# Performance work log

Hardware: AMD Instinct MI355X
Metric: run time of the kernel (lower is better)

## Reference

```python
import jax, jax.numpy as jnp
import numpy as np
from jax import lax

# db4 decomposition low-pass filter (pywt convention, ascending index)
DEC_LO = np.array([-0.010597401784997278, 0.032883011666982945, 0.030841381835986965,
                   -0.18703481171888114, -0.02798376941698385, 0.6308807679295904,
                   0.7148465705525415, 0.23037781330885523], dtype=np.float32)
L = 8
REC_LO = DEC_LO[::-1].copy()
DEC_HI = (REC_LO * ((-1.0) ** (np.arange(L) + 1))).astype(np.float32)
REC_HI = DEC_HI[::-1].copy()


def _dwt_last(x, lo, hi):
    """Single-level DWT along last axis, pywt 'symmetric' mode.
    Returns (cA, cD), each (..., (N+L-1)//2)."""
    ext = jnp.pad(x, [(0, 0)] * (x.ndim - 1) + [(L - 1, L - 1)], mode='symmetric')[..., 1:]
    z = ext.reshape(-1, 1, ext.shape[-1])
    # correlation with flipped filter == true convolution
    k = jnp.stack([lo[::-1], hi[::-1]])[:, None, :]  # (2,1,L)
    y = lax.conv_general_dilated(z, k, (2,), 'VALID', dimension_numbers=('NCH', 'OIH', 'NCH'))
    y = y.reshape(x.shape[:-1] + (2, y.shape[-1]))
    return y[..., 0, :], y[..., 1, :]


def _idwt_last(cA, cD, lo, hi):
    """Single-level inverse DWT along last axis (pywt upsampling convolution)."""
    n = cA.shape[-1]
    up = jnp.zeros(cA.shape[:-1] + (2, 2 * n - 1), cA.dtype)
    up = up.at[..., 0, ::2].set(cA).at[..., 1, ::2].set(cD)
    z = up.reshape(-1, 2, 2 * n - 1)
    k = jnp.stack([lo[::-1], hi[::-1]])[None, :, :]  # (1,2,L) -> sum of lo/hi branches
    y = lax.conv_general_dilated(z, k, (1,), [(L - 1, L - 1)], dimension_numbers=('NCH', 'OIH', 'NCH'))
    y = y[:, 0, L - 2: 2 * n]  # length 2n - L + 2
    return y.reshape(cA.shape[:-1] + (2 * n - L + 2,))


def dwt2d(x):
    lo, hi = jnp.asarray(DEC_LO), jnp.asarray(DEC_HI)
    a, d = _dwt_last(x, lo, hi)                       # along W
    aa, da = _dwt_last(a.swapaxes(-1, -2), lo, hi)    # along H
    ad, dd = _dwt_last(d.swapaxes(-1, -2), lo, hi)
    LL = aa.swapaxes(-1, -2)
    LH = da.swapaxes(-1, -2)   # cH: detail along H, approx along W
    HL = ad.swapaxes(-1, -2)   # cV: approx along H, detail along W
    HH = dd.swapaxes(-1, -2)
    return LL, LH, HL, HH


def idwt2d(LL, LH, HL, HH):
    lo, hi = jnp.asarray(REC_LO), jnp.asarray(REC_HI)
    a = _idwt_last(LL.swapaxes(-1, -2), LH.swapaxes(-1, -2), lo, hi).swapaxes(-1, -2)  # along H
    d = _idwt_last(HL.swapaxes(-1, -2), HH.swapaxes(-1, -2), lo, hi).swapaxes(-1, -2)
    return _idwt_last(a, d, lo, hi)  # along W


def attention_weight(x, c1w, c1b, c2w, gamma, beta, rmean, rvar):
    """x: (b, w, c, h). Max/mean pool over dim 1, 1x1 conv 2->1, depthwise conv1d
    over c channels, BatchNorm1d (eval), sigmoid gate."""
    feat = jnp.stack([x.max(axis=1), x.mean(axis=1)], axis=1)  # (b,2,c,h)
    y = jnp.einsum('i,bich->bch', c1w.reshape(2), feat) + c1b[0]  # (b,c,h)
    C = y.shape[1]
    p = (c2w.shape[-1] - 1) // 2
    y = lax.conv_general_dilated(y, c2w, (1,), [(p, p)], feature_group_count=C,
                                 dimension_numbers=('NCH', 'OIH', 'NCH'))
    y = (y - rmean[:, None]) * lax.rsqrt(rvar[:, None] + 1e-5) * gamma[:, None] + beta[:, None]
    return x * jax.nn.sigmoid(y)[:, None]


def _forward(x, lh_c1w, lh_c1b, lh_c2w, lh_g, lh_b, lh_m, lh_v,
             hl_c1w, hl_c1b, hl_c2w, hl_g, hl_b, hl_m, hl_v):
    LL, LH, HL, HH = dwt2d(x)
    LHp = attention_weight(LH.transpose(0, 3, 1, 2), lh_c1w, lh_c1b, lh_c2w, lh_g, lh_b, lh_m, lh_v).transpose(0, 2, 3, 1)
    HLp = attention_weight(HL.transpose(0, 2, 1, 3), hl_c1w, hl_c1b, hl_c2w, hl_g, hl_b, hl_m, hl_v).transpose(0, 2, 1, 3)
    rec = idwt2d(LL, LHp, HLp, HH)
    H, W = x.shape[-2], x.shape[-1]
    return x + rec[..., :H, :W]


def setup_inputs() -> dict:
    key = jax.random.key(0)
    ks = jax.random.split(key, 16)
    B, C, H, W, K = 8, 64, 512, 512, 3
    d = {"x": jax.random.normal(ks[0], (B, C, H, W), dtype=jnp.float32)}
    for i, pre in enumerate(["lh", "hl"]):
        base = 1 + 7 * i
        d[pre + "_c1w"] = jax.random.normal(ks[base + 0], (1, 2, 1, 1), dtype=jnp.float32) * 0.5
        d[pre + "_c1b"] = jax.random.normal(ks[base + 1], (1,), dtype=jnp.float32) * 0.1
        d[pre + "_c2w"] = jax.random.normal(ks[base + 2], (C, 1, K), dtype=jnp.float32) * 0.3
        d[pre + "_g"] = jnp.ones((C,), dtype=jnp.float32)
        d[pre + "_b"] = jnp.zeros((C,), dtype=jnp.float32)
        d[pre + "_m"] = jax.random.normal(ks[base + 3], (C,), dtype=jnp.float32) * 0.1
        d[pre + "_v"] = jax.random.uniform(ks[base + 4], (C,), dtype=jnp.float32, minval=0.5, maxval=1.5)
    return d


def reference(x, lh_c1w, lh_c1b, lh_c2w, lh_g, lh_b, lh_m, lh_v,
              hl_c1w, hl_c1b, hl_c2w, hl_g, hl_b, hl_m, hl_v):
    return _forward(x, lh_c1w, lh_c1b, lh_c2w, lh_g, lh_b, lh_m, lh_v,
                    hl_c1w, hl_c1b, hl_c2w, hl_g, hl_b, hl_m, hl_v)
```

## Files before the change

### kernel.cpp

```cpp
#include <hip/hip_runtime.h>

typedef _Float16 h16;
typedef _Float16 h16x4 __attribute__((ext_vector_type(4)));
typedef _Float16 h16x8 __attribute__((ext_vector_type(8)));
typedef float f32x4 __attribute__((ext_vector_type(4)));

#define N_IMG 512
#define C_CH  64
#define H_IN  512
#define W_IN  512
#define NC    259
#define PIT   260
#define PITH  264
#define S_IMGH ((size_t)NC * PITH)
#define NSB    ((size_t)N_IMG * S_IMGH)
#define GPIT  264
#define NSTRIP 33

constexpr float DLO[8] = {
  -0.010597401784997278f,  0.032883011666982945f,  0.030841381835986965f, -0.18703481171888114f,
  -0.02798376941698385f,   0.6308807679295904f,    0.7148465705525415f,    0.23037781330885523f};
constexpr float DHI[8] = {
  -0.23037781330885523f,   0.7148465705525415f,   -0.6308807679295904f,   -0.02798376941698385f,
   0.18703481171888114f,   0.030841381835986965f, -0.032883011666982945f, -0.010597401784997278f};
constexpr float RLO[8] = {
   0.23037781330885523f,   0.7148465705525415f,    0.6308807679295904f,   -0.02798376941698385f,
  -0.18703481171888114f,   0.030841381835986965f,  0.032883011666982945f, -0.010597401784997278f};
constexpr float RHI[8] = {
  -0.010597401784997278f, -0.032883011666982945f,  0.030841381835986965f,  0.18703481171888114f,
  -0.02798376941698385f,  -0.6308807679295904f,    0.7148465705525415f,   -0.23037781330885523f};

__global__ __launch_bounds__(512) void k_fwd(const float* __restrict__ x,
                                             h16* __restrict__ wsh,
                                             float* __restrict__ stat) {
  __shared__ float sa[22 * PIT];
  __shared__ float sd[22 * PIT];
  const int p = blockIdx.x;
  const int w = (p & 7) * 2112 + (p >> 3);
  const int bc = w / NSTRIP;
  const int bx = w - bc * NSTRIP;
  const int h0 = bx * 8;
  const int hcount = min(8, NC - h0);
  const int nrows = 2 * hcount + 6;
  const int tid = threadIdx.x;
  const int wave = tid >> 6, lane = tid & 63;
  const float* xim = x + (size_t)bc * (H_IN * (size_t)W_IN);

  for (int j = wave; j < nrows; j += 8) {
    int r = 2 * h0 - 6 + j;
    r = r < 0 ? -r - 1 : (r >= H_IN ? 2 * H_IN - 1 - r : r);
    const float* xrow = xim + (size_t)r * W_IN;
    float* saj = sa + j * PIT;
    float* sdj = sd + j * PIT;
    const int base = lane ? 8 * lane - 8 : 0;
    const float4 q0 = *(const float4*)(xrow + base);
    const float4 q1 = *(const float4*)(xrow + base + 4);
    const float4 q2 = *(const float4*)(xrow + base + 8);
    const float4 q3 = *(const float4*)(xrow + base + 12);
    const float v[16] = {q0.x, q0.y, q0.z, q0.w, q1.x, q1.y, q1.z, q1.w,
                         q2.x, q2.y, q2.z, q2.w, q3.x, q3.y, q3.z, q3.w};
    float A[4], D[4];
    if (lane == 0) {
#pragma unroll
      for (int i = 0; i < 4; ++i) {
        float a = 0.f, d = 0.f;
#pragma unroll
        for (int m = 0; m < 8; ++m) {
          int pp = 2 * i + 1 - m; pp = pp < 0 ? -pp - 1 : pp;
          const float t = v[pp];
          a += DLO[m] * t; d += DHI[m] * t;
        }
        A[i] = a; D[i] = d;
      }
      *(float4*)(saj) = {A[0], A[1], A[2], A[3]};
      *(float4*)(sdj) = {D[0], D[1], D[2], D[3]};
    } else {
#pragma unroll
      for (int k = 0; k < 4; ++k) {
        float a = 0.f, d = 0.f;
#pragma unroll
        for (int m = 0; m < 8; ++m) {
          const float t = v[2 * k + 9 - m];
          a += DLO[m] * t; d += DHI[m] * t;
        }
        A[k] = a; D[k] = d;
      }
      *(float4*)(saj + 4 * lane) = {A[0], A[1], A[2], A[3]};
      *(float4*)(sdj + 4 * lane) = {D[0], D[1], D[2], D[3]};
      if (lane == 63) {
#pragma unroll
        for (int i = 256; i < 259; ++i) {
          float a = 0.f, d = 0.f;
#pragma unroll
          for (int m = 0; m < 8; ++m) {
            int pp = 2 * i + 1 - m; pp = pp >= 512 ? 1023 - pp : pp;
            const float t = v[pp - 496];
            a += DLO[m] * t; d += DHI[m] * t;
          }
          saj[i] = a; sdj[i] = d;
        }
      }
    }
  }
  __syncthreads();

  h16* __restrict__ LHp = wsh;
  h16* __restrict__ HLp = wsh + NSB;
  const size_t obase = (size_t)bc * S_IMGH;
  const int ntask = hcount * 65;
  float rlh[2][4], rhl[2][4];
#pragma unroll
  for (int slot = 0; slot < 2; ++slot) {
    const int task = tid + slot * 512;
    if (task < ntask) {
      const int dh = task / 65, pq = task - dh * 65;
      const int i0 = 4 * pq;
      float lh[4] = {0, 0, 0, 0}, hl[4] = {0, 0, 0, 0};
#pragma unroll
      for (int m = 0; m < 8; ++m) {
        const int j = 2 * dh + 7 - m;
        const float4 av = *(const float4*)(sa + j * PIT + i0);
        const float4 dv = *(const float4*)(sd + j * PIT + i0);
        lh[0] += DHI[m] * av.x; lh[1] += DHI[m] * av.y; lh[2] += DHI[m] * av.z; lh[3] += DHI[m] * av.w;
        hl[0] += DLO[m] * dv.x; hl[1] += DLO[m] * dv.y; hl[2] += DLO[m] * dv.z; hl[3] += DLO[m] * dv.w;
      }
      if (i0 == 256) { lh[3] = 0.f; hl[3] = 0.f; }
      const size_t ob = obase + (size_t)(h0 + dh) * PITH + i0;
      h16x4 o;
      o[0] = (h16)lh[0]; o[1] = (h16)lh[1]; o[2] = (h16)lh[2]; o[3] = (h16)lh[3];
      *(h16x4*)(LHp + ob) = o;
      o[0] = (h16)hl[0]; o[1] = (h16)hl[1]; o[2] = (h16)hl[2]; o[3] = (h16)hl[3];
      *(h16x4*)(HLp + ob) = o;
#pragma unroll
      for (int k = 0; k < 4; ++k) { rlh[slot][k] = lh[k]; rhl[slot][k] = hl[k]; }
    }
  }
  __syncthreads();

  float* scol = sa;
  float* prmx = sa + 8 * 264;
  float* prsm = prmx + 520;
#pragma unroll
  for (int slot = 0; slot < 2; ++slot) {
    const int task = tid + slot * 512;
    if (task < ntask) {
      const int dh = task / 65, pq = task - dh * 65;
      *(float4*)(scol + dh * 264 + 4 * pq) = {rhl[slot][0], rhl[slot][1], rhl[slot][2], rhl[slot][3]};
      const float m01 = fmaxf(rlh[slot][0], rlh[slot][1]);
      const float m23 = (pq == 64) ? rlh[slot][2] : fmaxf(rlh[slot][2], rlh[slot][3]);
      prmx[task] = fmaxf(m01, m23);
      prsm[task] = rlh[slot][0] + rlh[slot][1] + rlh[slot][2] + rlh[slot][3];
    }
  }
  __syncthreads();
  float* rsM = stat;
  float* rsS = stat + (size_t)N_IMG * 264;
  float* cpM = rsS + (size_t)N_IMG * 264;
  float* cpS = cpM + (size_t)N_IMG * NSTRIP * 264;
  if (wave < hcount) {
    float m = prmx[wave * 65 + lane], s = prsm[wave * 65 + lane];
    if (lane == 0) { m = fmaxf(m, prmx[wave * 65 + 64]); s += prsm[wave * 65 + 64]; }
#pragma unroll
    for (int off = 32; off; off >>= 1) {
      m = fmaxf(m, __shfl_xor(m, off)); s += __shfl_xor(s, off);
    }
    if (lane == 0) {
      rsM[bc * 264 + h0 + wave] = m;
      rsS[bc * 264 + h0 + wave] = s;
    }
  }
  if (tid < 264) {
    float m = -3.4e38f, s = 0.f;
    for (int dh = 0; dh < hcount; ++dh) {
      const float vv = scol[dh * 264 + tid]; m = fmaxf(m, vv); s += vv;
    }
    const size_t cb = ((size_t)bc * NSTRIP + bx) * 264 + tid;
    cpM[cb] = m; cpS[cb] = s;
  }
}

__global__ __launch_bounds__(256) void k_gate(
    const float* __restrict__ stat, float* __restrict__ gout,
    const float* lc1w, const float* lc1b, const float* lc2w,
    const float* lg, const float* lb, const float* lm, const float* lv,
    const float* hc1w, const float* hc1b, const float* hc2w,
    const float* hg, const float* hb, const float* hm, const float* hv) {
  __shared__ float cmx[264], csm[264], y0a[264], y0b[264];
  const int bc = blockIdx.x;
  const int tid = threadIdx.x;
  const float* rsM = stat;
  const float* rsS = stat + (size_t)N_IMG * 264;
  const float* cpM = rsS + (size_t)N_IMG * 264;
  const float* cpS = cpM + (size_t)N_IMG * NSTRIP * 264;

  for (int col = tid; col < 264; col += 256) {
    float m = -3.4e38f, s = 0.f;
    for (int st = 0; st < NSTRIP; ++st) {
      const size_t cb = ((size_t)bc * NSTRIP + st) * 264 + col;
      m = fmaxf(m, cpM[cb]); s += cpS[cb];
    }
    cmx[col] = m; csm[col] = s;
  }
  __syncthreads();
  const float lw0 = lc1w[0], lw1 = lc1w[1], lbb0 = lc1b[0];
  const float hw0 = hc1w[0], hw1 = hc1w[1], hbb0 = hc1b[0];
  for (int idx = tid; idx < NC; idx += 256) {
    y0a[idx] = lw0 * rsM[bc * 264 + idx] + lw1 * (rsS[bc * 264 + idx] * (1.f / NC)) + lbb0;
    y0b[idx] = hw0 * cmx[idx] + hw1 * (csm[idx] * (1.f / NC)) + hbb0;
  }
  __syncthreads();
  const int c = bc & (C_CH - 1);
  const float lk0 = lc2w[c * 3], lk1 = lc2w[c * 3 + 1], lk2 = lc2w[c * 3 + 2];
  const float hk0 = hc2w[c * 3], hk1 = hc2w[c * 3 + 1], hk2 = hc2w[c * 3 + 2];
  const float lsc = rsqrtf(lv[c] + 1e-5f) * lg[c], lmu = lm[c], lbe = lb[c];
  const float hsc = rsqrtf(hv[c] + 1e-5f) * hg[c], hmu = hm[c], hbe = hb[c];
  for (int idx = tid; idx < NC; idx += 256) {
    float a = idx > 0 ? y0a[idx - 1] : 0.f;
    float b = y0a[idx];
    float d = idx < NC - 1 ? y0a[idx + 1] : 0.f;
    float y = lk0 * a + lk1 * b + lk2 * d;
    y = (y - lmu) * lsc + lbe;
    gout[(size_t)bc * GPIT + idx] = 1.f / (1.f + expf(-y)) - 1.f;

    a = idx > 0 ? y0b[idx - 1] : 0.f;
    b = y0b[idx];
    d = idx < NC - 1 ? y0b[idx + 1] : 0.f;
    y = hk0 * a + hk1 * b + hk2 * d;
    y = (y - hmu) * hsc + hbe;
    gout[(size_t)N_IMG * GPIT + (size_t)bc * GPIT + idx] = 1.f / (1.f + expf(-y)) - 1.f;
  }
}

__global__ __launch_bounds__(512) void k_inv(const h16* __restrict__ wsh,
                                             const float* __restrict__ gbuf,
                                             const float* __restrict__ x,
                                             float* __restrict__ out) {
  __shared__ float sB[7][PITH], sC[7][PITH];
  __shared__ float a2[8][PITH], d2[8][PITH];
  __shared__ float sghl[PITH];
  const int p = blockIdx.x;
  const int w = (p & 7) * 4096 + (p >> 3);
  const int bc = w >> 6;
  const int t0 = (w & 63) * 8;
  const int u0 = t0 >> 1;
  const int tid = threadIdx.x;
  const h16* LHh = wsh       + (size_t)bc * S_IMGH;
  const h16* HLh = wsh + NSB + (size_t)bc * S_IMGH;
  const float* glh = gbuf + (size_t)bc * GPIT;
  const float* ghl = gbuf + (size_t)N_IMG * GPIT + (size_t)bc * GPIT;

  if (tid < 66) *(float4*)(sghl + 4 * tid) = *(const float4*)(ghl + 4 * tid);

  for (int q = tid; q < 7 * 33; q += 512) {
    const int j = q / 33, b8 = (q - j * 33) * 8;
    const int u = u0 + j;
    const float gl = glh[u];
    const size_t rb = (size_t)u * PITH + b8;
    const h16x8 Bv = *(const h16x8*)(LHh + rb);
    const h16x8 Cv = *(const h16x8*)(HLh + rb);
    float4 f0 = {(float)Bv[0] * gl, (float)Bv[1] * gl, (float)Bv[2] * gl, (float)Bv[3] * gl};
    float4 f1 = {(float)Bv[4] * gl, (float)Bv[5] * gl, (float)Bv[6] * gl, (float)Bv[7] * gl};
    *(float4*)(&sB[j][b8]) = f0; *(float4*)(&sB[j][b8 + 4]) = f1;
    f0 = {(float)Cv[0], (float)Cv[1], (float)Cv[2], (float)Cv[3]};
    f1 = {(float)Cv[4], (float)Cv[5], (float)Cv[6], (float)Cv[7]};
    *(float4*)(&sC[j][b8]) = f0; *(float4*)(&sC[j][b8 + 4]) = f1;
  }
  __syncthreads();

  for (int task = tid; task < 8 * 132; task += 512) {
    const int dt = task / 132, pq = task - dt * 132;
    const int i = 2 * pq;
    const int par = dt & 1, lj0 = dt >> 1;
    float ax = 0.f, ay = 0.f, dx_ = 0.f, dy_ = 0.f;
#pragma unroll
    for (int jj = 0; jj < 4; ++jj) {
      const int lj = lj0 + 3 - jj;
      const float rh = par ? RHI[1 + 2 * jj] : RHI[2 * jj];
      const float rl = par ? RLO[1 + 2 * jj] : RLO[2 * jj];
      const float2 b_ = *(const float2*)(&sB[lj][i]);
      const float2 c_ = *(const float2*)(&sC[lj][i]);
      ax += b_.x * rh; ay += b_.y * rh;
      dx_ += c_.x * rl; dy_ += c_.y * rl;
    }
    *(float2*)(&a2[dt][i]) = {ax, ay};
    *(float2*)(&d2[dt][i]) = {sghl[i] * dx_, sghl[i + 1] * dy_};
  }
  __syncthreads();

  for (int task = tid; task < 8 * 128; task += 512) {
    const int dt = task >> 7, r = task & 127;
    const int q = 2 * r;
    const float a_[5] = {a2[dt][q], a2[dt][q + 1], a2[dt][q + 2], a2[dt][q + 3], a2[dt][q + 4]};
    const float d_[5] = {d2[dt][q], d2[dt][q + 1], d2[dt][q + 2], d2[dt][q + 3], d2[dt][q + 4]};
    float vv[4];
#pragma unroll
    for (int k = 0; k < 4; ++k) {
      float s = 0.f;
      const int base = k >> 1, par = k & 1;
#pragma unroll
      for (int jj = 0; jj < 4; ++jj)
        s += a_[base + 3 - jj] * RLO[par + 2 * jj] + d_[base + 3 - jj] * RHI[par + 2 * jj];
      vv[k] = s;
    }
    const size_t orow = ((size_t)bc * H_IN + (size_t)(t0 + dt)) * W_IN + 4 * r;
    const f32x4 xv = __builtin_nontemporal_load((const f32x4*)(x + orow));
    f32x4 ov;
    ov.x = 2.f * xv.x + vv[0]; ov.y = 2.f * xv.y + vv[1];
    ov.z = 2.f * xv.z + vv[2]; ov.w = 2.f * xv.w + vv[3];
    __builtin_nontemporal_store(ov, (f32x4*)(out + orow));
  }
}

extern "C" void kernel_launch(void* const* d_in, const int* in_sizes, int n_in,
                              void* d_out, int out_size, void* d_ws, size_t ws_size,
                              hipStream_t stream) {
  const float* x = (const float*)d_in[0];
  h16* wsh = (h16*)d_ws;
  float* statf = (float*)(wsh + 2 * NSB);
  float* gbuf = statf + 2 * (size_t)N_IMG * 264 + 2 * (size_t)N_IMG * NSTRIP * 264;
  float* out = (float*)d_out;

  k_fwd<<<dim3(NSTRIP * N_IMG), 512, 0, stream>>>(x, wsh, statf);
  k_gate<<<dim3(N_IMG), 256, 0, stream>>>(
      statf, gbuf,
      (const float*)d_in[1], (const float*)d_in[2], (const float*)d_in[3],
      (const float*)d_in[4], (const float*)d_in[5], (const float*)d_in[6], (const float*)d_in[7],
      (const float*)d_in[8], (const float*)d_in[9], (const float*)d_in[10],
      (const float*)d_in[11], (const float*)d_in[12], (const float*)d_in[13], (const float*)d_in[14]);
  k_inv<<<dim3(64 * N_IMG), 512, 0, stream>>>(wsh, gbuf, x, out);
}
```

Measured before the change: 437.6 us.

## Double k_inv row tile and read fp16 subbands directly from global memory

k_inv now handles 16 output rows per block instead of 8, which halves the grid and reduces how often the overlapping subband rows are reloaded between neighbouring tiles. The shared-memory staging of the LH/HL rows and the HL gate is removed. Threads now read fp16 pairs straight from global memory and fold the LH gate into the filter coefficient, which removes one sync and one LDS pass. The cost is narrow 4-byte global loads, repeated across threads and taps and relying on cache hits, in place of 16-byte coalesced staging. There is also less parallelism per launch.

```diff
diff --git a/kernel.cpp b/kernel.cpp
--- a/kernel.cpp
+++ b/kernel.cpp
@@ -1,6 +1,7 @@
 #include <hip/hip_runtime.h>
 
 typedef _Float16 h16;
+typedef _Float16 h16x2 __attribute__((ext_vector_type(2)));
 typedef _Float16 h16x4 __attribute__((ext_vector_type(4)));
 typedef _Float16 h16x8 __attribute__((ext_vector_type(8)));
 typedef float f32x4 __attribute__((ext_vector_type(4)));
@@ -235,13 +236,11 @@
                                              const float* __restrict__ gbuf,
                                              const float* __restrict__ x,
                                              float* __restrict__ out) {
-  __shared__ float sB[7][PITH], sC[7][PITH];
-  __shared__ float a2[8][PITH], d2[8][PITH];
-  __shared__ float sghl[PITH];
+  __shared__ float a2[16][PITH], d2[16][PITH];
   const int p = blockIdx.x;
-  const int w = (p & 7) * 4096 + (p >> 3);
-  const int bc = w >> 6;
-  const int t0 = (w & 63) * 8;
+  const int w = (p & 7) * 2048 + (p >> 3);
+  const int bc = w >> 5;
+  const int t0 = (w & 31) * 16;
   const int u0 = t0 >> 1;
   const int tid = threadIdx.x;
   const h16* LHh = wsh       + (size_t)bc * S_IMGH;
@@ -249,45 +248,29 @@
   const float* glh = gbuf + (size_t)bc * GPIT;
   const float* ghl = gbuf + (size_t)N_IMG * GPIT + (size_t)bc * GPIT;
 
-  if (tid < 66) *(float4*)(sghl + 4 * tid) = *(const float4*)(ghl + 4 * tid);
-
-  for (int q = tid; q < 7 * 33; q += 512) {
-    const int j = q / 33, b8 = (q - j * 33) * 8;
-    const int u = u0 + j;
-    const float gl = glh[u];
-    const size_t rb = (size_t)u * PITH + b8;
-    const h16x8 Bv = *(const h16x8*)(LHh + rb);
-    const h16x8 Cv = *(const h16x8*)(HLh + rb);
-    float4 f0 = {(float)Bv[0] * gl, (float)Bv[1] * gl, (float)Bv[2] * gl, (float)Bv[3] * gl};
-    float4 f1 = {(float)Bv[4] * gl, (float)Bv[5] * gl, (float)Bv[6] * gl, (float)Bv[7] * gl};
-    *(float4*)(&sB[j][b8]) = f0; *(float4*)(&sB[j][b8 + 4]) = f1;
-    f0 = {(float)Cv[0], (float)Cv[1], (float)Cv[2], (float)Cv[3]};
-    f1 = {(float)Cv[4], (float)Cv[5], (float)Cv[6], (float)Cv[7]};
-    *(float4*)(&sC[j][b8]) = f0; *(float4*)(&sC[j][b8 + 4]) = f1;
-  }
-  __syncthreads();
-
-  for (int task = tid; task < 8 * 132; task += 512) {
+  for (int task = tid; task < 16 * 132; task += 512) {
     const int dt = task / 132, pq = task - dt * 132;
     const int i = 2 * pq;
     const int par = dt & 1, lj0 = dt >> 1;
     float ax = 0.f, ay = 0.f, dx_ = 0.f, dy_ = 0.f;
 #pragma unroll
     for (int jj = 0; jj < 4; ++jj) {
-      const int lj = lj0 + 3 - jj;
-      const float rh = par ? RHI[1 + 2 * jj] : RHI[2 * jj];
+      const int u = u0 + lj0 + 3 - jj;
+      const float rhg = (par ? RHI[1 + 2 * jj] : RHI[2 * jj]) * glh[u];
       const float rl = par ? RLO[1 + 2 * jj] : RLO[2 * jj];
-      const float2 b_ = *(const float2*)(&sB[lj][i]);
-      const float2 c_ = *(const float2*)(&sC[lj][i]);
-      ax += b_.x * rh; ay += b_.y * rh;
-      dx_ += c_.x * rl; dy_ += c_.y * rl;
-    }
+      const size_t rb = (size_t)u * PITH + i;
+      const h16x2 bv = *(const h16x2*)(LHh + rb);
+      const h16x2 cv = *(const h16x2*)(HLh + rb);
+      ax += (float)bv[0] * rhg; ay += (float)bv[1] * rhg;
+      dx_ += (float)cv[0] * rl; dy_ += (float)cv[1] * rl;
+    }
+    const float2 gh = *(const float2*)(ghl + i);
     *(float2*)(&a2[dt][i]) = {ax, ay};
-    *(float2*)(&d2[dt][i]) = {sghl[i] * dx_, sghl[i + 1] * dy_};
-  }
-  __syncthreads();
-
-  for (int task = tid; task < 8 * 128; task += 512) {
+    *(float2*)(&d2[dt][i]) = {gh.x * dx_, gh.y * dy_};
+  }
+  __syncthreads();
+
+  for (int task = tid; task < 16 * 128; task += 512) {
     const int dt = task >> 7, r = task & 127;
     const int q = 2 * r;
     const float a_[5] = {a2[dt][q], a2[dt][q + 1], a2[dt][q + 2], a2[dt][q + 3], a2[dt][q + 4]};
@@ -327,5 +310,5 @@
       (const float*)d_in[4], (const float*)d_in[5], (const float*)d_in[6], (const float*)d_in[7],
       (const float*)d_in[8], (const float*)d_in[9], (const float*)d_in[10],
       (const float*)d_in[11], (const float*)d_in[12], (const float*)d_in[13], (const float*)d_in[14]);
-  k_inv<<<dim3(64 * N_IMG), 512, 0, stream>>>(wsh, gbuf, x, out);
+  k_inv<<<dim3(32 * N_IMG), 512, 0, stream>>>(wsh, gbuf, x, out);
 }
```

New measurement: 464.0 us. 6.0% more time.
